# Performance work log

Hardware: AMD Instinct MI355X
Metric: run time of the kernel (lower is better)

Reference implementation:

```python
import jax, jax.numpy as jnp
import numpy as np

N, D, C = 65536, 512, 10000

def setup_inputs() -> dict:
    key = jax.random.key(0)
    k1, k2, k3 = jax.random.split(key, 3)
    feature = jax.random.normal(k1, (N, D), dtype=jnp.float32)
    label = jax.random.randint(k2, (N,), 0, C, dtype=jnp.int64)
    center_vector = jax.random.normal(k3, (C, D), dtype=jnp.float32)
    return {"feature": feature, "label": label, "center_vector": center_vector, "class_num": C}

def reference(feature, label, center_vector, class_num):
    # Original loop over class_num: for each class j, mask = (label==j); the
    # masked term norm((feature*mask - center[j]) * mask, dim=1) is zero for
    # samples whose label != j, so the accumulated per-sample value is exactly
    # ||feature_i - center_vector[label_i]||_2. Loop collapses to one gather.
    diff = feature - center_vector[label]            # [N, D]
    per_sample = jnp.linalg.norm(diff, axis=1)       # [N]
    loss = per_sample.sum() / feature.shape[0]
    return loss
```

## Files before the change

### kernel.cpp

```cpp
#include <hip/hip_runtime.h>


#define N_SAMPLES 65536
#define DIM 512
#define GRID_BLOCKS 2048
#define BLOCK_THREADS 256
#define WAVES_PER_BLOCK 4
#define TOTAL_WAVES (GRID_BLOCKS * WAVES_PER_BLOCK)

__global__ __launch_bounds__(BLOCK_THREADS) void center_loss_pass1(
    const float* __restrict__ feature,
    const int* __restrict__ label,
    const float* __restrict__ center,
    float* __restrict__ partial) {
    __shared__ float wsum[WAVES_PER_BLOCK];

    const int wave = threadIdx.x >> 6;
    const int lane = threadIdx.x & 63;
    const int gwave0 = blockIdx.x * WAVES_PER_BLOCK + wave;

    float acc = 0.0f;

    for (int s = gwave0; s < N_SAMPLES; s += TOTAL_WAVES) {
        const int lab = label[s];
        const float4* fp = reinterpret_cast<const float4*>(feature + (size_t)s * DIM) + lane * 2;
        const float4* cp = reinterpret_cast<const float4*>(center + (size_t)lab * DIM) + lane * 2;
        const float4 f0 = fp[0];
        const float4 f1 = fp[1];
        const float4 c0 = cp[0];
        const float4 c1 = cp[1];

        float ss = 0.0f, d;
        d = f0.x - c0.x; ss = fmaf(d, d, ss);
        d = f0.y - c0.y; ss = fmaf(d, d, ss);
        d = f0.z - c0.z; ss = fmaf(d, d, ss);
        d = f0.w - c0.w; ss = fmaf(d, d, ss);
        d = f1.x - c1.x; ss = fmaf(d, d, ss);
        d = f1.y - c1.y; ss = fmaf(d, d, ss);
        d = f1.z - c1.z; ss = fmaf(d, d, ss);
        d = f1.w - c1.w; ss = fmaf(d, d, ss);

        #pragma unroll
        for (int off = 32; off > 0; off >>= 1)
            ss += __shfl_xor(ss, off, 64);

        if (lane == 0)
            acc += sqrtf(ss);
    }

    if (lane == 0) wsum[wave] = acc;
    __syncthreads();
    if (threadIdx.x == 0)
        partial[blockIdx.x] = wsum[0] + wsum[1] + wsum[2] + wsum[3];
}

__global__ __launch_bounds__(BLOCK_THREADS) void center_loss_pass2(
    const float* __restrict__ partial,
    float* __restrict__ out) {
    __shared__ float lds[WAVES_PER_BLOCK];
    const int wave = threadIdx.x >> 6;
    const int lane = threadIdx.x & 63;

    float s = 0.0f;
    for (int i = threadIdx.x; i < GRID_BLOCKS; i += BLOCK_THREADS)
        s += partial[i];

    #pragma unroll
    for (int off = 32; off > 0; off >>= 1)
        s += __shfl_xor(s, off, 64);

    if (lane == 0) lds[wave] = s;
    __syncthreads();
    if (threadIdx.x == 0)
        out[0] = (lds[0] + lds[1] + lds[2] + lds[3]) * (1.0f / (float)N_SAMPLES);
}

extern "C" void kernel_launch(void* const* d_in, const int* in_sizes, int n_in,
                              void* d_out, int out_size, void* d_ws, size_t ws_size,
                              hipStream_t stream) {
    const float* feature = (const float*)d_in[0];
    const int*   label   = (const int*)d_in[1];
    const float* center  = (const float*)d_in[2];
    float* out = (float*)d_out;
    float* partial = (float*)d_ws;

    center_loss_pass1<<<GRID_BLOCKS, BLOCK_THREADS, 0, stream>>>(feature, label, center, partial);
    center_loss_pass2<<<1, BLOCK_THREADS, 0, stream>>>(partial, out);
}
```

Baseline: 45.26 us.

## Assign contiguous samples per wave, prefetch next row, batch shuffle reductions

Each wave now handles a contiguous run of samples instead of a grid-strided set. Labels are preloaded into registers and the next sample's feature and center rows are software-prefetched while the current one is computed. Feature loads use nontemporal hints to avoid polluting cache. The cross-lane shuffle reductions are deferred and interleaved across all samples to expose more ILP, at the cost of higher register use.

```diff
diff --git a/kernel.cpp b/kernel.cpp
--- a/kernel.cpp
+++ b/kernel.cpp
@@ -1,12 +1,16 @@
 #include <hip/hip_runtime.h>
 
 
+typedef float f32x4 __attribute__((ext_vector_type(4)));
+
 #define N_SAMPLES 65536
 #define DIM 512
+#define F4_PER_ROW (DIM / 4)
 #define GRID_BLOCKS 2048
 #define BLOCK_THREADS 256
 #define WAVES_PER_BLOCK 4
 #define TOTAL_WAVES (GRID_BLOCKS * WAVES_PER_BLOCK)
+#define SPW (N_SAMPLES / TOTAL_WAVES)
 
 __global__ __launch_bounds__(BLOCK_THREADS) void center_loss_pass1(
     const float* __restrict__ feature,
@@ -17,38 +21,67 @@
 
     const int wave = threadIdx.x >> 6;
     const int lane = threadIdx.x & 63;
-    const int gwave0 = blockIdx.x * WAVES_PER_BLOCK + wave;
+    const int gw = blockIdx.x * WAVES_PER_BLOCK + wave;
+    const int s0 = gw * SPW;
 
-    float acc = 0.0f;
+    int labs[SPW];
+    const int* lp = label + s0;
+    #pragma unroll
+    for (int k = 0; k < SPW; ++k) labs[k] = lp[k];
 
-    for (int s = gwave0; s < N_SAMPLES; s += TOTAL_WAVES) {
-        const int lab = label[s];
-        const float4* fp = reinterpret_cast<const float4*>(feature + (size_t)s * DIM) + lane * 2;
-        const float4* cp = reinterpret_cast<const float4*>(center + (size_t)lab * DIM) + lane * 2;
-        const float4 f0 = fp[0];
-        const float4 f1 = fp[1];
-        const float4 c0 = cp[0];
-        const float4 c1 = cp[1];
+    const f32x4* fb = reinterpret_cast<const f32x4*>(feature)
+                      + (size_t)s0 * F4_PER_ROW + lane * 2;
+    const f32x4* cbase = reinterpret_cast<const f32x4*>(center);
 
-        float ss = 0.0f, d;
-        d = f0.x - c0.x; ss = fmaf(d, d, ss);
-        d = f0.y - c0.y; ss = fmaf(d, d, ss);
-        d = f0.z - c0.z; ss = fmaf(d, d, ss);
-        d = f0.w - c0.w; ss = fmaf(d, d, ss);
-        d = f1.x - c1.x; ss = fmaf(d, d, ss);
-        d = f1.y - c1.y; ss = fmaf(d, d, ss);
-        d = f1.z - c1.z; ss = fmaf(d, d, ss);
-        d = f1.w - c1.w; ss = fmaf(d, d, ss);
+    float ss[SPW];
 
-        #pragma unroll
-        for (int off = 32; off > 0; off >>= 1)
-            ss += __shfl_xor(ss, off, 64);
+    f32x4 f0c = __builtin_nontemporal_load(fb);
+    f32x4 f1c = __builtin_nontemporal_load(fb + 1);
+    const f32x4* cp0 = cbase + (size_t)labs[0] * F4_PER_ROW + lane * 2;
+    f32x4 c0c = cp0[0];
+    f32x4 c1c = cp0[1];
 
-        if (lane == 0)
-            acc += sqrtf(ss);
+    #pragma unroll
+    for (int k = 0; k < SPW; ++k) {
+        f32x4 f0n, f1n, c0n, c1n;
+        if (k < SPW - 1) {
+            const f32x4* fn = fb + (size_t)(k + 1) * F4_PER_ROW;
+            f0n = __builtin_nontemporal_load(fn);
+            f1n = __builtin_nontemporal_load(fn + 1);
+            const f32x4* cn = cbase + (size_t)labs[k + 1] * F4_PER_ROW + lane * 2;
+            c0n = cn[0];
+            c1n = cn[1];
+        }
+
+        float s = 0.0f, d;
+        d = f0c.x - c0c.x; s = fmaf(d, d, s);
+        d = f0c.y - c0c.y; s = fmaf(d, d, s);
+        d = f0c.z - c0c.z; s = fmaf(d, d, s);
+        d = f0c.w - c0c.w; s = fmaf(d, d, s);
+        d = f1c.x - c1c.x; s = fmaf(d, d, s);
+        d = f1c.y - c1c.y; s = fmaf(d, d, s);
+        d = f1c.z - c1c.z; s = fmaf(d, d, s);
+        d = f1c.w - c1c.w; s = fmaf(d, d, s);
+        ss[k] = s;
+
+        if (k < SPW - 1) {
+            f0c = f0n; f1c = f1n; c0c = c0n; c1c = c1n;
+        }
     }
 
-    if (lane == 0) wsum[wave] = acc;
+    #pragma unroll
+    for (int off = 32; off > 0; off >>= 1) {
+        #pragma unroll
+        for (int k = 0; k < SPW; ++k)
+            ss[k] += __shfl_xor(ss[k], off, 64);
+    }
+
+    if (lane == 0) {
+        float a = 0.0f;
+        #pragma unroll
+        for (int k = 0; k < SPW; ++k) a += sqrtf(ss[k]);
+        wsum[wave] = a;
+    }
     __syncthreads();
     if (threadIdx.x == 0)
         partial[blockIdx.x] = wsum[0] + wsum[1] + wsum[2] + wsum[3];
```

New measurement: 53.33 us. +17.9%, slower.

## Fuse final reduction via last-block atomic counter and use nontemporal feature loads

Applied to the files above, without the earlier changes.

Merges the two-pass reduction into one kernel: each block writes its partial sum, increments an atomic counter, and the last block to finish reduces all partials and writes the loss. Feature rows are read with nontemporal loads so they stream past the cache and leave room for reused center rows. This drops the second kernel launch but adds a memset launch for the counter, plus a fence and an atomic per block.

```diff
diff --git a/kernel.cpp b/kernel.cpp
--- a/kernel.cpp
+++ b/kernel.cpp
@@ -1,34 +1,42 @@
 #include <hip/hip_runtime.h>
 
 
+typedef float f32x4 __attribute__((ext_vector_type(4)));
+
 #define N_SAMPLES 65536
 #define DIM 512
+#define F4_PER_ROW (DIM / 4)
 #define GRID_BLOCKS 2048
 #define BLOCK_THREADS 256
 #define WAVES_PER_BLOCK 4
 #define TOTAL_WAVES (GRID_BLOCKS * WAVES_PER_BLOCK)
 
-__global__ __launch_bounds__(BLOCK_THREADS) void center_loss_pass1(
+__global__ __launch_bounds__(BLOCK_THREADS) void center_loss_fused(
     const float* __restrict__ feature,
     const int* __restrict__ label,
     const float* __restrict__ center,
-    float* __restrict__ partial) {
+    float* __restrict__ out,
+    float* __restrict__ partial,
+    unsigned int* __restrict__ done) {
     __shared__ float wsum[WAVES_PER_BLOCK];
+    __shared__ int amLast;
 
     const int wave = threadIdx.x >> 6;
     const int lane = threadIdx.x & 63;
-    const int gwave0 = blockIdx.x * WAVES_PER_BLOCK + wave;
+    const int gw = blockIdx.x * WAVES_PER_BLOCK + wave;
 
     float acc = 0.0f;
 
-    for (int s = gwave0; s < N_SAMPLES; s += TOTAL_WAVES) {
+    for (int s = gw; s < N_SAMPLES; s += TOTAL_WAVES) {
         const int lab = label[s];
-        const float4* fp = reinterpret_cast<const float4*>(feature + (size_t)s * DIM) + lane * 2;
-        const float4* cp = reinterpret_cast<const float4*>(center + (size_t)lab * DIM) + lane * 2;
-        const float4 f0 = fp[0];
-        const float4 f1 = fp[1];
-        const float4 c0 = cp[0];
-        const float4 c1 = cp[1];
+        const f32x4* fp = reinterpret_cast<const f32x4*>(feature)
+                          + (size_t)s * F4_PER_ROW + lane * 2;
+        const f32x4* cp = reinterpret_cast<const f32x4*>(center)
+                          + (size_t)lab * F4_PER_ROW + lane * 2;
+        const f32x4 f0 = __builtin_nontemporal_load(fp);
+        const f32x4 f1 = __builtin_nontemporal_load(fp + 1);
+        const f32x4 c0 = cp[0];
+        const f32x4 c1 = cp[1];
 
         float ss = 0.0f, d;
         d = f0.x - c0.x; ss = fmaf(d, d, ss);
@@ -50,29 +58,27 @@
 
     if (lane == 0) wsum[wave] = acc;
     __syncthreads();
-    if (threadIdx.x == 0)
+    if (threadIdx.x == 0) {
         partial[blockIdx.x] = wsum[0] + wsum[1] + wsum[2] + wsum[3];
-}
+        __threadfence();
+        unsigned int prev = atomicAdd(done, 1u);
+        amLast = (prev == GRID_BLOCKS - 1) ? 1 : 0;
+    }
+    __syncthreads();
 
-__global__ __launch_bounds__(BLOCK_THREADS) void center_loss_pass2(
-    const float* __restrict__ partial,
-    float* __restrict__ out) {
-    __shared__ float lds[WAVES_PER_BLOCK];
-    const int wave = threadIdx.x >> 6;
-    const int lane = threadIdx.x & 63;
-
-    float s = 0.0f;
-    for (int i = threadIdx.x; i < GRID_BLOCKS; i += BLOCK_THREADS)
-        s += partial[i];
-
-    #pragma unroll
-    for (int off = 32; off > 0; off >>= 1)
-        s += __shfl_xor(s, off, 64);
-
-    if (lane == 0) lds[wave] = s;
-    __syncthreads();
-    if (threadIdx.x == 0)
-        out[0] = (lds[0] + lds[1] + lds[2] + lds[3]) * (1.0f / (float)N_SAMPLES);
+    if (amLast) {
+        __threadfence();
+        float s2 = 0.0f;
+        for (int i = threadIdx.x; i < GRID_BLOCKS; i += BLOCK_THREADS)
+            s2 += partial[i];
+        #pragma unroll
+        for (int off = 32; off > 0; off >>= 1)
+            s2 += __shfl_xor(s2, off, 64);
+        if (lane == 0) wsum[wave] = s2;
+        __syncthreads();
+        if (threadIdx.x == 0)
+            out[0] = (wsum[0] + wsum[1] + wsum[2] + wsum[3]) * (1.0f / (float)N_SAMPLES);
+    }
 }
 
 extern "C" void kernel_launch(void* const* d_in, const int* in_sizes, int n_in,
@@ -83,7 +89,10 @@
     const float* center  = (const float*)d_in[2];
     float* out = (float*)d_out;
     float* partial = (float*)d_ws;
+    unsigned int* done = (unsigned int*)((char*)d_ws + GRID_BLOCKS * sizeof(float));
 
-    center_loss_pass1<<<GRID_BLOCKS, BLOCK_THREADS, 0, stream>>>(feature, label, center, partial);
-    center_loss_pass2<<<1, BLOCK_THREADS, 0, stream>>>(partial, out);
+    hipMemsetAsync((void*)done, 0, sizeof(unsigned int), stream);
+
+    center_loss_fused<<<GRID_BLOCKS, BLOCK_THREADS, 0, stream>>>(
+        feature, label, center, out, partial, done);
 }
```

New measurement: 144.0 us. 218% more time.
